# Kernel tuning notes

Hardware: AMD Instinct MI355X
Metric: run time of the kernel (lower is better)

The kernel has to match this reference:

```python
import jax, jax.numpy as jnp
import numpy as np

N = 100000        # nodes
E = 3200000       # edges (avg degree 32)
NFEAT = 512
NHID = 256
NCLASS = 64
NLAYERS = 8
TAU = 0.5


def setup_inputs() -> dict:
    key = jax.random.key(0)
    ks = jax.random.split(key, 9)
    X = jax.random.normal(ks[0], (N, NFEAT), dtype=jnp.float32)
    edge_row = jax.random.randint(ks[1], (E,), 0, N, dtype=jnp.int32)
    edge_col = jax.random.randint(ks[2], (E,), 0, N, dtype=jnp.int32)
    # edge weights ~ 1/avg_degree so spmm is roughly norm-preserving (like a normalized adjacency)
    edge_w = jax.random.uniform(ks[3], (E,), dtype=jnp.float32) / 16.0
    W_init = jax.random.normal(ks[4], (NFEAT, NHID), dtype=jnp.float32) / np.sqrt(NFEAT).astype(np.float32)
    b_init = jnp.zeros((NHID,), dtype=jnp.float32)
    # original reset_parameters zeroes gamma and W; use small random values so the
    # computation is numerically non-trivial (same math either way)
    gammas = jax.random.normal(ks[5], (NLAYERS,), dtype=jnp.float32) * 0.1
    Ws = jax.random.normal(ks[6], (NLAYERS, NHID, NHID), dtype=jnp.float32) / np.sqrt(NHID).astype(np.float32)
    W_sort = jax.random.normal(ks[7], (NHID, NCLASS), dtype=jnp.float32) / np.sqrt(NHID).astype(np.float32)
    b_sort = jnp.zeros((NCLASS,), dtype=jnp.float32)
    return {"X": X, "edge_row": edge_row, "edge_col": edge_col, "edge_w": edge_w,
            "W_init": W_init, "b_init": b_init, "gammas": gammas, "Ws": Ws,
            "W_sort": W_sort, "b_sort": b_sort}


def reference(X, edge_row, edge_col, edge_w, W_init, b_init, gammas, Ws, W_sort, b_sort):
    # eval mode: F.dropout is identity
    H = X @ W_init + b_init                      # [N, NHID] init_dim_reduction
    I = jnp.eye(NHID, dtype=H.dtype)
    betas = TAU / jnp.arange(1, NLAYERS + 1, dtype=H.dtype)

    def spmm(M):
        # out[i] = sum_{e: row[e]=i} w[e] * M[col[e]]
        return jax.ops.segment_sum(edge_w[:, None] * M[edge_col], edge_row, num_segments=N)

    def step(carry, inp):
        Xc, acc = carry
        gamma, W, beta = inp
        AX = spmm(Xc)                             # sparse A @ X
        acc = acc + AX @ ((1.0 - beta) * I + beta * W)
        Xn = gamma * (Xc - AX)                    # next_x for the following layer
        return (Xn, acc), None

    (_, outputs), _ = jax.lax.scan(step, (H, H), (gammas, Ws, betas))
    return jax.nn.log_softmax(outputs @ W_sort + b_sort, axis=1)
```

## Files before the change

### kernel.cpp

```cpp
#include <hip/hip_runtime.h>

#define NNODES 100000
#define NEDGES 3200000
#define NFEAT  512
#define NHID   256
#define NCLS   64
#define NLAYERS 8
#define SCAN_NB ((NNODES + 1023) / 1024)

typedef short s8v __attribute__((ext_vector_type(8)));
typedef unsigned short u8v __attribute__((ext_vector_type(8)));
typedef unsigned int u4v __attribute__((ext_vector_type(4)));
typedef float f4v __attribute__((ext_vector_type(4)));
typedef float f2v __attribute__((ext_vector_type(2)));

__device__ __forceinline__ float bf2f(unsigned short u) {
    union { unsigned int i; float f; } v; v.i = ((unsigned int)u) << 16; return v.f;
}
__device__ __forceinline__ unsigned short f2bf(float f) {
    union { float f; unsigned int u; } v; v.f = f;
    unsigned int u = v.u;
    u += 0x7FFFu + ((u >> 16) & 1u);
    return (unsigned short)(u >> 16);
}
__device__ __forceinline__ float ldf(const void* p, size_t i, int f32) {
    return f32 ? ((const float*)p)[i] : bf2f(((const unsigned short*)p)[i]);
}
__device__ __forceinline__ int em_col(long long m) { return (int)(unsigned int)m; }
__device__ __forceinline__ float em_w(long long m) {
    union { int i; float f; } u; u.i = (int)((unsigned long long)m >> 32); return u.f;
}
__device__ __forceinline__ f2v ex2(unsigned int v) {
    union { unsigned int u; float f; } lo, hi;
    lo.u = v << 16; hi.u = v & 0xFFFF0000u;
    return (f2v){lo.f, hi.f};
}
#define SW(off, row) ((off) ^ (((row) & 7) << 4))

__global__ void probe_kernel(const unsigned short* __restrict__ ew, int* __restrict__ flag) {
    int i = threadIdx.x;
    unsigned short v = ew[2 * i];
    bool bad = (v & 0x8000u) || (v > 0x3D80u);
    unsigned long long m = __ballot(bad);
    if (i == 0) *flag = (m != 0ull) ? 1 : 0;
}

__global__ void hist_kernel(const int* __restrict__ row, int* __restrict__ counts) {
    int e = blockIdx.x * 256 + threadIdx.x;
    if (e < NEDGES) atomicAdd(&counts[row[e]], 1);
}

__global__ void scan_local(const int* __restrict__ counts, int* __restrict__ row_ptr,
                           int* __restrict__ bsum) {
    __shared__ int lds[1024];
    const int tid = threadIdx.x;
    const int i = blockIdx.x * 1024 + tid;
    int v = (i < NNODES) ? counts[i] : 0;
    lds[tid] = v;
    __syncthreads();
    for (int off = 1; off < 1024; off <<= 1) {
        int t = (tid >= off) ? lds[tid - off] : 0;
        __syncthreads();
        lds[tid] += t;
        __syncthreads();
    }
    if (i < NNODES) row_ptr[i] = lds[tid] - v;
    if (tid == 1023) bsum[blockIdx.x] = lds[1023];
}

__global__ void scan_bsum(int* __restrict__ bsum) {
    if (threadIdx.x == 0) {
        int acc = 0;
        for (int i = 0; i < SCAN_NB; ++i) { int v = bsum[i]; bsum[i] = acc; acc += v; }
        bsum[SCAN_NB] = acc;
    }
}

__global__ void scan_add(int* __restrict__ row_ptr, int* __restrict__ cursor,
                         const int* __restrict__ bsum) {
    const int i = blockIdx.x * 1024 + threadIdx.x;
    if (i < NNODES) {
        int v = row_ptr[i] + bsum[blockIdx.x];
        row_ptr[i] = v;
        cursor[i]  = v;
    }
    if (i == NNODES) row_ptr[NNODES] = bsum[SCAN_NB];
}

__global__ void scatter_kernel(const int* __restrict__ row, const int* __restrict__ col,
                               const void* __restrict__ w, int* __restrict__ cursor,
                               long long* __restrict__ em,
                               const int* __restrict__ flagp) {
    const int f32 = *flagp;
    int e = blockIdx.x * 256 + threadIdx.x;
    if (e < NEDGES) {
        int r = row[e];
        int pos = atomicAdd(&cursor[r], 1);
        float wv = ldf(w, e, f32);
        union { float f; unsigned int u; } uw; uw.f = wv;
        long long rec = ((long long)uw.u << 32) | (unsigned int)col[e];
        em[pos] = rec;
    }
}

template<int K, int N>
__global__ void pack_b(const void* __restrict__ src, unsigned short* __restrict__ dst,
                       const int* __restrict__ flagp) {
    const int f32 = *flagp;
    const int NT = N / 16;
    const int total = (K / 32) * NT * 64;
    int tid = blockIdx.x * 256 + threadIdx.x;
    if (tid >= total) return;
    int lane = tid & 63, rest = tid >> 6;
    int nt = rest % NT, ks = rest / NT;
    int n  = nt * 16 + (lane & 15);
    int kb = ks * 32 + (lane >> 4) * 8;
    unsigned short tmp[8];
#pragma unroll
    for (int j = 0; j < 8; ++j) tmp[j] = f2bf(ldf(src, (size_t)(kb + j) * N + n, f32));
#pragma unroll
    for (int j = 0; j < 8; ++j) dst[(size_t)tid * 8 + j] = tmp[j];
}

__global__ void pack_wcomb(const void* __restrict__ Ws, const void* __restrict__ Wsort,
                           unsigned short* __restrict__ dst, const int* __restrict__ flagp) {
    const int f32 = *flagp;
    int tid = blockIdx.x * 256 + threadIdx.x;
    if (tid >= 16384) return;
    int lane = tid & 63;
    int rest = tid >> 6;
    int nt = rest & 3;
    int ks = (rest >> 2) & 7;
    int l  = rest >> 5;
    int n  = nt * 16 + (lane & 15);
    int kb = ks * 32 + (lane >> 4) * 8;
    float beta = 0.5f / (float)(l + 1);
    float ombeta = 1.0f - beta;
    const size_t wl = (size_t)l * NHID * NHID;
    unsigned short tmp[8];
#pragma unroll
    for (int j = 0; j < 8; ++j) {
        int k = kb + j;
        float s = 0.0f;
        for (int q = 0; q < NHID; ++q)
            s = fmaf(ldf(Ws, wl + (size_t)k * NHID + q, f32),
                     ldf(Wsort, (size_t)q * NCLS + n, f32), s);
        tmp[j] = f2bf(ombeta * ldf(Wsort, (size_t)k * NCLS + n, f32) + beta * s);
    }
#pragma unroll
    for (int j = 0; j < 8; ++j) dst[(size_t)tid * 8 + j] = tmp[j];
}

template<int K, int NTT, int NTW, int MT, bool SHARE, bool ADYN, bool ACCUM, bool BIAS, bool OUTBF>
__global__ __launch_bounds__(256) void gemm_mfma(
    const void* __restrict__ Av, const s8v* __restrict__ Bp,
    const void* __restrict__ bias,
    float* __restrict__ Cf, unsigned short* __restrict__ Cb,
    const int* __restrict__ flagp)
{
    const int f32 = (ADYN || BIAS) ? *flagp : 0;
    const int N    = NTT * 16;
    const int lane = threadIdx.x & 63;
    const int wid  = threadIdx.x >> 6;
    int mbase, nt0;
    if (SHARE) {
        mbase = blockIdx.x * (MT * 16);
        nt0   = wid * NTW;
    } else {
        const int job = blockIdx.x * 4 + wid;
        mbase = job * (MT * 16);
        nt0   = 0;
    }
    if (mbase >= NNODES) return;
    const int l15  = lane & 15;
    const int quad = lane >> 4;

    f4v acc[MT][NTW];
#pragma unroll
    for (int mt = 0; mt < MT; ++mt)
#pragma unroll
        for (int nt = 0; nt < NTW; ++nt)
            acc[mt][nt] = (f4v){0.f, 0.f, 0.f, 0.f};

#pragma unroll 4
    for (int ks = 0; ks < K / 32; ++ks) {
        const int kb = ks * 32 + quad * 8;
        s8v a[MT];
        if (ADYN && f32) {
            const float* Af = (const float*)Av;
#pragma unroll
            for (int mt = 0; mt < MT; ++mt) {
                const float4* p = (const float4*)(Af + (size_t)(mbase + mt * 16 + l15) * K + kb);
                float4 x0 = p[0], x1 = p[1];
                a[mt][0] = (short)f2bf(x0.x); a[mt][1] = (short)f2bf(x0.y);
                a[mt][2] = (short)f2bf(x0.z); a[mt][3] = (short)f2bf(x0.w);
                a[mt][4] = (short)f2bf(x1.x); a[mt][5] = (short)f2bf(x1.y);
                a[mt][6] = (short)f2bf(x1.z); a[mt][7] = (short)f2bf(x1.w);
            }
        } else {
            const unsigned short* A = (const unsigned short*)Av;
#pragma unroll
            for (int mt = 0; mt < MT; ++mt)
                a[mt] = *(const s8v*)(A + (size_t)(mbase + mt * 16 + l15) * K + kb);
        }
#pragma unroll
        for (int nt = 0; nt < NTW; ++nt) {
            s8v b = Bp[(ks * NTT + nt0 + nt) * 64 + lane];
#pragma unroll
            for (int mt = 0; mt < MT; ++mt)
                acc[mt][nt] = __builtin_amdgcn_mfma_f32_16x16x32_bf16(a[mt], b, acc[mt][nt], 0, 0, 0);
        }
    }

#pragma unroll
    for (int mt = 0; mt < MT; ++mt) {
#pragma unroll
        for (int nt = 0; nt < NTW; ++nt) {
#pragma unroll
            for (int r = 0; r < 4; ++r) {
                int row = mbase + mt * 16 + quad * 4 + r;
                int col = (nt0 + nt) * 16 + l15;
                float v = acc[mt][nt][r];
                if (BIAS) v += ldf(bias, col, f32);
                size_t idx = (size_t)row * N + col;
                if (OUTBF) {
                    Cb[idx] = f2bf(v);
                } else {
                    if (ACCUM) v += Cf[idx];
                    Cf[idx] = v;
                }
            }
        }
    }
}

template<bool FIRST, bool LAST>
__global__ __launch_bounds__(256) void spmm_fused(
    const int* __restrict__ row_ptr, const long long* __restrict__ em,
    const unsigned short* __restrict__ Xc, unsigned short* __restrict__ Xn,
    const s8v* __restrict__ WcombL, const s8v* __restrict__ WsortP,
    const void* __restrict__ bsort, float* __restrict__ Zacc,
    const void* __restrict__ gammas, int layer, const int* __restrict__ flagp)
{
    __shared__ unsigned short axl[16 * 256];
    __shared__ unsigned short hxl[FIRST ? 16 * 256 : 4];
    const int wid  = threadIdx.x >> 6;
    const int lane = threadIdx.x & 63;
    const int half = lane >> 5;
    const int l32  = lane & 31;
    const int mbase = blockIdx.x * 16;
    const int f32 = *flagp;
    const float g = LAST ? 0.f : ldf(gammas, layer, f32);

    for (int s = 0; s < 4; ++s) {
        const int row  = wid * 4 + s;
        const int node = mbase + row;
        const int start = row_ptr[node];
        const int end   = row_ptr[node + 1];
        f2v acc[4];
#pragma unroll
        for (int k = 0; k < 4; ++k) acc[k] = (f2v){0.f, 0.f};

        int e = start;
        for (; e + 16 <= end; e += 16) {
            long long m[8];
#pragma unroll
            for (int j = 0; j < 8; ++j) m[j] = em[e + 2 * j + half];
            u8v q[8];
#pragma unroll
            for (int j = 0; j < 8; ++j)
                q[j] = *(const u8v*)(Xc + (size_t)em_col(m[j]) * NHID + l32 * 8);
#pragma unroll
            for (int j = 0; j < 8; ++j) {
                float w = em_w(m[j]);
                f2v wv = (f2v){w, w};
                u4v qw = __builtin_bit_cast(u4v, q[j]);
#pragma unroll
                for (int k = 0; k < 4; ++k) acc[k] += wv * ex2(qw[k]);
            }
        }
        for (; e + 2 <= end; e += 2) {
            long long m = em[e + half];
            float w = em_w(m);
            f2v wv = (f2v){w, w};
            u8v q = *(const u8v*)(Xc + (size_t)em_col(m) * NHID + l32 * 8);
            u4v qw = __builtin_bit_cast(u4v, q);
#pragma unroll
            for (int k = 0; k < 4; ++k) acc[k] += wv * ex2(qw[k]);
        }
        if (e < end) {
            long long m = em[e];
            float w = half ? 0.f : em_w(m);
            f2v wv = (f2v){w, w};
            u8v q = *(const u8v*)(Xc + (size_t)em_col(m) * NHID + l32 * 8);
            u4v qw = __builtin_bit_cast(u4v, q);
#pragma unroll
            for (int k = 0; k < 4; ++k) acc[k] += wv * ex2(qw[k]);
        }

        float a[8];
#pragma unroll
        for (int k = 0; k < 4; ++k) { a[2 * k] = acc[k].x; a[2 * k + 1] = acc[k].y; }
#pragma unroll
        for (int i = 0; i < 8; ++i) a[i] += __shfl_xor(a[i], 32, 64);

        const int loff = SW(row * 512 + l32 * 16, row);
        if (half == 0) {
            u8v ov;
#pragma unroll
            for (int i = 0; i < 8; ++i) ov[i] = f2bf(a[i]);
            *(u8v*)((char*)axl + loff) = ov;
        } else if (FIRST || !LAST) {
            u8v xi = *(const u8v*)(Xc + (size_t)node * NHID + l32 * 8);
            if constexpr (FIRST)
                *(u8v*)((char*)hxl + loff) = xi;
            if constexpr (!LAST) {
                u8v xn;
#pragma unroll
                for (int i = 0; i < 8; ++i) xn[i] = f2bf(g * (bf2f(xi[i]) - a[i]));
                *(u8v*)(Xn + (size_t)node * NHID + l32 * 8) = xn;
            }
        }
    }
    __syncthreads();

    const int l15  = lane & 15;
    const int quad = lane >> 4;
    f4v gacc = (f4v){0.f, 0.f, 0.f, 0.f};
#pragma unroll
    for (int ks = 0; ks < NHID / 32; ++ks) {
        const int boff = SW(l15 * 512 + ks * 64 + quad * 16, l15);
        s8v av = *(const s8v*)((const char*)axl + boff);
        s8v b = WcombL[(ks * 4 + wid) * 64 + lane];
        gacc = __builtin_amdgcn_mfma_f32_16x16x32_bf16(av, b, gacc, 0, 0, 0);
        if constexpr (FIRST) {
            s8v h  = *(const s8v*)((const char*)hxl + boff);
            s8v b2 = WsortP[(ks * 4 + wid) * 64 + lane];
            gacc = __builtin_amdgcn_mfma_f32_16x16x32_bf16(h, b2, gacc, 0, 0, 0);
        }
    }
#pragma unroll
    for (int r = 0; r < 4; ++r) {
        const int orow = mbase + quad * 4 + r;
        const int col = wid * 16 + l15;
        const size_t idx = (size_t)orow * NCLS + col;
        float v = gacc[r];
        if constexpr (FIRST) Zacc[idx] = v + ldf(bsort, col, f32);
        else                 Zacc[idx] += v;
    }
}

__global__ __launch_bounds__(256) void lsm_kernel(const float* __restrict__ Z,
                                                  void* __restrict__ out,
                                                  const int* __restrict__ flagp) {
    const int f32 = *flagp;
    const int wid  = threadIdx.x >> 6;
    const int lane = threadIdx.x & 63;
    const int row  = blockIdx.x * 4 + wid;
    if (row >= NNODES) return;
    float z = Z[(size_t)row * NCLS + lane];
    float m = z;
#pragma unroll
    for (int off = 32; off >= 1; off >>= 1) m = fmaxf(m, __shfl_xor(m, off, 64));
    float s = __expf(z - m);
#pragma unroll
    for (int off = 32; off >= 1; off >>= 1) s += __shfl_xor(s, off, 64);
    float r = z - m - __logf(s);
    size_t idx = (size_t)row * NCLS + lane;
    if (f32) ((float*)out)[idx] = r;
    else     ((unsigned short*)out)[idx] = f2bf(r);
}

extern "C" void kernel_launch(void* const* d_in, const int* in_sizes, int n_in,
                              void* d_out, int out_size, void* d_ws, size_t ws_size,
                              hipStream_t stream)
{
    const void* X      = d_in[0];
    const int*  erow   = (const int*)d_in[1];
    const int*  ecol   = (const int*)d_in[2];
    const void* ew     = d_in[3];
    const void* Winit  = d_in[4];
    const void* binit  = d_in[5];
    const void* gammas = d_in[6];
    const void* Ws     = d_in[7];
    const void* Wsort  = d_in[8];
    const void* bsort  = d_in[9];

    char* p = (char*)d_ws;
    auto alloc = [&](size_t bytes) -> char* {
        char* r = p; p += (bytes + 255) & ~(size_t)255; return r;
    };
    int*            flag   = (int*)           alloc(256);
    float*          Zacc   = (float*)         alloc((size_t)NNODES * NCLS * 4);
    unsigned short* Xc0    = (unsigned short*)alloc((size_t)NNODES * NHID * 2);
    unsigned short* Xc1    = (unsigned short*)alloc((size_t)NNODES * NHID * 2);
    int*            counts = (int*)           alloc((size_t)(NNODES + 1) * 4);
    int*            row_ptr= (int*)           alloc((size_t)(NNODES + 1) * 4);
    int*            cursor = (int*)           alloc((size_t)(NNODES + 1) * 4);
    int*            bsum   = (int*)           alloc((size_t)(SCAN_NB + 1) * 4);
    long long*      em     = (long long*)     alloc((size_t)NEDGES * 8);
    unsigned short* WinitP = (unsigned short*)alloc((size_t)NFEAT * NHID * 2);
    unsigned short* WsortP = (unsigned short*)alloc((size_t)NHID * NCLS * 2);
    unsigned short* WcombP = (unsigned short*)alloc((size_t)NLAYERS * NHID * NCLS * 2);

    probe_kernel<<<1, 64, 0, stream>>>((const unsigned short*)ew, flag);

    hipMemsetAsync(counts, 0, (size_t)NNODES * 4, stream);
    hist_kernel<<<NEDGES / 256, 256, 0, stream>>>(erow, counts);
    scan_local<<<SCAN_NB, 1024, 0, stream>>>(counts, row_ptr, bsum);
    scan_bsum<<<1, 64, 0, stream>>>(bsum);
    scan_add<<<SCAN_NB, 1024, 0, stream>>>(row_ptr, cursor, bsum);
    scatter_kernel<<<NEDGES / 256, 256, 0, stream>>>(erow, ecol, ew, cursor, em, flag);

    pack_b<NFEAT, NHID><<<64, 256, 0, stream>>>(Winit, WinitP, flag);
    pack_b<NHID, NCLS><<<8, 256, 0, stream>>>(Wsort, WsortP, flag);
    pack_wcomb<<<64, 256, 0, stream>>>(Ws, Wsort, WcombP, flag);

    gemm_mfma<NFEAT, 16, 4, 2, true, true, false, true, true>
        <<<NNODES / 32, 256, 0, stream>>>(X, (const s8v*)WinitP, binit, nullptr, Xc0, flag);

    unsigned short* cur = Xc0;
    unsigned short* nxt = Xc1;
    const int fgrid = NNODES / 16;
    for (int l = 0; l < NLAYERS; ++l) {
        const s8v* Wl = (const s8v*)WcombP + (size_t)l * 2048;
        if (l == 0)
            spmm_fused<true, false><<<fgrid, 256, 0, stream>>>(
                row_ptr, em, cur, nxt, Wl, (const s8v*)WsortP, bsort, Zacc, gammas, l, flag);
        else if (l < NLAYERS - 1)
            spmm_fused<false, false><<<fgrid, 256, 0, stream>>>(
                row_ptr, em, cur, nxt, Wl, (const s8v*)WsortP, bsort, Zacc, gammas, l, flag);
        else
            spmm_fused<false, true><<<fgrid, 256, 0, stream>>>(
                row_ptr, em, cur, nxt, Wl, (const s8v*)WsortP, bsort, Zacc, gammas, l, flag);
        unsigned short* t = cur; cur = nxt; nxt = t;
    }

    lsm_kernel<<<NNODES / 4, 256, 0, stream>>>(Zacc, d_out, flag);
}
```

Before: 2.836 ms.

## Split edge scatter into row-range passes and use nontemporal streaming loads

The CSR scatter now runs as four passes, each handling only edges whose destination row lies in a quarter of the node range. This keeps the cursor atomics and em writes of each pass within a smaller, more cache-resident region. Edge row, column and weight reads, plus the em record reads in the SpMM loop, now use nontemporal loads so streaming data is less likely to evict reused feature rows. The cost is that the row array is read four times, along with four extra kernel launches.

```diff
diff --git a/kernel.cpp b/kernel.cpp
--- a/kernel.cpp
+++ b/kernel.cpp
@@ -7,6 +7,7 @@
 #define NCLS   64
 #define NLAYERS 8
 #define SCAN_NB ((NNODES + 1023) / 1024)
+#define SC_NPASS 4
 
 typedef short s8v __attribute__((ext_vector_type(8)));
 typedef unsigned short u8v __attribute__((ext_vector_type(8)));
@@ -47,7 +48,7 @@
 
 __global__ void hist_kernel(const int* __restrict__ row, int* __restrict__ counts) {
     int e = blockIdx.x * 256 + threadIdx.x;
-    if (e < NEDGES) atomicAdd(&counts[row[e]], 1);
+    if (e < NEDGES) atomicAdd(&counts[__builtin_nontemporal_load(row + e)], 1);
 }
 
 __global__ void scan_local(const int* __restrict__ counts, int* __restrict__ row_ptr,
@@ -87,20 +88,24 @@
     if (i == NNODES) row_ptr[NNODES] = bsum[SCAN_NB];
 }
 
-__global__ void scatter_kernel(const int* __restrict__ row, const int* __restrict__ col,
-                               const void* __restrict__ w, int* __restrict__ cursor,
-                               long long* __restrict__ em,
-                               const int* __restrict__ flagp) {
+__global__ __launch_bounds__(256) void scatter_pass(
+    const int* __restrict__ row, const int* __restrict__ col,
+    const void* __restrict__ w, int* __restrict__ cursor,
+    long long* __restrict__ em, const int* __restrict__ flagp,
+    int lo, int hi)
+{
     const int f32 = *flagp;
     int e = blockIdx.x * 256 + threadIdx.x;
-    if (e < NEDGES) {
-        int r = row[e];
-        int pos = atomicAdd(&cursor[r], 1);
-        float wv = ldf(w, e, f32);
-        union { float f; unsigned int u; } uw; uw.f = wv;
-        long long rec = ((long long)uw.u << 32) | (unsigned int)col[e];
-        em[pos] = rec;
-    }
+    if (e >= NEDGES) return;
+    int r = __builtin_nontemporal_load(row + e);
+    if (r < lo || r >= hi) return;
+    int c = __builtin_nontemporal_load(col + e);
+    float wv = f32 ? __builtin_nontemporal_load((const float*)w + e)
+                   : bf2f(__builtin_nontemporal_load((const unsigned short*)w + e));
+    union { float f; unsigned int u; } uw; uw.f = wv;
+    long long rec = ((long long)uw.u << 32) | (unsigned int)c;
+    int pos = atomicAdd(&cursor[r], 1);
+    em[pos] = rec;
 }
 
 template<int K, int N>
@@ -265,7 +270,7 @@
         for (; e + 16 <= end; e += 16) {
             long long m[8];
 #pragma unroll
-            for (int j = 0; j < 8; ++j) m[j] = em[e + 2 * j + half];
+            for (int j = 0; j < 8; ++j) m[j] = __builtin_nontemporal_load(&em[e + 2 * j + half]);
             u8v q[8];
 #pragma unroll
             for (int j = 0; j < 8; ++j)
@@ -280,7 +285,7 @@
             }
         }
         for (; e + 2 <= end; e += 2) {
-            long long m = em[e + half];
+            long long m = __builtin_nontemporal_load(&em[e + half]);
             float w = em_w(m);
             f2v wv = (f2v){w, w};
             u8v q = *(const u8v*)(Xc + (size_t)em_col(m) * NHID + l32 * 8);
@@ -289,7 +294,7 @@
             for (int k = 0; k < 4; ++k) acc[k] += wv * ex2(qw[k]);
         }
         if (e < end) {
-            long long m = em[e];
+            long long m = __builtin_nontemporal_load(&em[e]);
             float w = half ? 0.f : em_w(m);
             f2v wv = (f2v){w, w};
             u8v q = *(const u8v*)(Xc + (size_t)em_col(m) * NHID + l32 * 8);
@@ -410,7 +415,10 @@
     scan_local<<<SCAN_NB, 1024, 0, stream>>>(counts, row_ptr, bsum);
     scan_bsum<<<1, 64, 0, stream>>>(bsum);
     scan_add<<<SCAN_NB, 1024, 0, stream>>>(row_ptr, cursor, bsum);
-    scatter_kernel<<<NEDGES / 256, 256, 0, stream>>>(erow, ecol, ew, cursor, em, flag);
+    for (int pass = 0; pass < SC_NPASS; ++pass)
+        scatter_pass<<<NEDGES / 256, 256, 0, stream>>>(
+            erow, ecol, ew, cursor, em, flag,
+            pass * (NNODES / SC_NPASS), (pass + 1) * (NNODES / SC_NPASS));
 
     pack_b<NFEAT, NHID><<<64, 256, 0, stream>>>(Winit, WinitP, flag);
     pack_b<NHID, NCLS><<<8, 256, 0, stream>>>(Wsort, WsortP, flag);
```

Measured after the change: 2.867 ms. Within noise of the previous version (+1.1%).
